# Performance work log

Hardware: AMD Instinct MI355X
Metric: run time of the kernel (lower is better)

The kernel has to match this reference:

```python
import jax, jax.numpy as jnp
import numpy as np

NUM_HEADS = 12
EPS = 1e-6


def softmax_with_policy(attn, policy, eps=EPS):
    # attn: [B, H, N, N]; policy: [B, N, 1]
    B, H, N, _ = attn.shape
    attn_policy = policy.reshape(B, 1, 1, N)
    eye = jnp.eye(N, dtype=attn_policy.dtype).reshape(1, 1, N, N)
    attn_policy = attn_policy + (1.0 - attn_policy) * eye
    max_att = jnp.max(attn, axis=-1, keepdims=True)
    a = jnp.exp((attn - max_att).astype(jnp.float32)) * attn_policy.astype(jnp.float32)
    a = (a + eps / N) / (jnp.sum(a, axis=-1, keepdims=True) + eps)
    return a.astype(attn.dtype)


def setup_inputs() -> dict:
    key = jax.random.key(0)
    k1, k2, k3 = jax.random.split(key, 3)
    B, N, C = 16, 1024, 768
    x = jax.random.normal(k1, (B, N, C), dtype=jnp.float32)
    policy = jax.random.uniform(k2, (B, N, 1), dtype=jnp.float32)
    w_qkv = jax.random.normal(k3, (3 * C, C), dtype=jnp.float32) * (C ** -0.5)
    w_proj = jax.random.normal(jax.random.fold_in(key, 7), (C, C), dtype=jnp.float32) * (C ** -0.5)
    b_proj = jnp.zeros((C,), dtype=jnp.float32)
    return {"x": x, "policy": policy, "w_qkv": w_qkv, "w_proj": w_proj, "b_proj": b_proj, "sampler": 0}


def reference(x, policy, w_qkv, w_proj, b_proj, sampler):
    B, N, C = x.shape
    H = NUM_HEADS
    hd = C // H
    scale = hd ** -0.5
    qkv = (x @ w_qkv.T).reshape(B, N, 3, H, hd)
    qkv = jnp.transpose(qkv, (2, 0, 3, 1, 4))  # [3, B, H, N, hd]
    q, k, v = qkv[0], qkv[1], qkv[2]
    attn = jnp.einsum('bhnd,bhmd->bhnm', q, k) * scale
    attn = softmax_with_policy(attn, policy)
    out = jnp.einsum('bhnm,bhmd->bhnd', attn, v)
    out = jnp.transpose(out, (0, 2, 1, 3)).reshape(B, N, C)
    return out @ w_proj.T + b_proj
```

## Files before the change

kernel.cpp:

```cpp
#include <hip/hip_runtime.h>


#define NB 16
#define NN 1024
#define NC 768
#define NH 12
#define HD 64
#define NM (NB*NN)
#define QKVC (3*NC)
#define QSCALE 0.18033688011112042f
#define PSTR 68

typedef _Float16 f16;
typedef _Float16 f16x8 __attribute__((ext_vector_type(8)));
typedef _Float16 f16x4 __attribute__((ext_vector_type(4)));
typedef __fp16 fp16x2 __attribute__((ext_vector_type(2)));
typedef float f32x4 __attribute__((ext_vector_type(4)));

#if __has_builtin(__builtin_amdgcn_exp2f)
#define EXP2(x) __builtin_amdgcn_exp2f(x)
#else
#define EXP2(x) exp2f(x)
#endif

#define MFMA16(a,b,c) __builtin_amdgcn_mfma_f32_16x16x32_f16((a),(b),(c),0,0,0)
#define SCHED_FENCE() __builtin_amdgcn_sched_barrier(0)

__device__ inline f16x8 as_f16x8(uint4 u){
  union { uint4 u; f16x8 h; } v; v.u = u; return v.h;
}

__device__ inline void gl_lds16(const f16* g, f16* l){
  __builtin_amdgcn_global_load_lds(
      (const __attribute__((address_space(1))) void*)g,
      (__attribute__((address_space(3))) void*)l, 16, 0, 0);
}

#define CVT_N1 (NM*NC/4)
#define CVT_N2 (QKVC*NC/4)
#define CVT_N3 (NC*NC/4)
__global__ void cvt_all(const float* __restrict__ x, const float* __restrict__ wq,
                        const float* __restrict__ wp, f16* __restrict__ xh,
                        f16* __restrict__ wqh, f16* __restrict__ wph){
  int i = blockIdx.x*blockDim.x + threadIdx.x;
  const float* in; f16* out; int j;
  if (i < CVT_N1){ in = x; out = xh; j = i; }
  else if (i < CVT_N1 + CVT_N2){ in = wq; out = wqh; j = i - CVT_N1; }
  else { in = wp; out = wph; j = i - CVT_N1 - CVT_N2; }
  float4 v = ((const float4*)in)[j];
  f16x4 h; h[0]=(f16)v.x; h[1]=(f16)v.y; h[2]=(f16)v.z; h[3]=(f16)v.w;
  ((f16x4*)out)[j] = h;
}

#define GEMM_STAGE(SRC_A, SRC_B, BUF, BK)                                     \
  _Pragma("unroll")                                                           \
  for (int r = 0; r < 2; r++){                                                \
    int row = r*64 + row0;                                                    \
    gl_lds16(SRC_A + (size_t)(R0 + row)*NC + (BK) + kc0, sA[BUF] + r*2048 + w*512); \
    gl_lds16(SRC_B + (size_t)(C0 + row)*NC + (BK) + kc0, sB[BUF] + r*2048 + w*512); \
  }

#define GEMM_PIPELINE(SRC_A, SRC_B)                                           \
  GEMM_STAGE(SRC_A, SRC_B, 0, 0);                                             \
  GEMM_STAGE(SRC_A, SRC_B, 1, 32);                                            \
  _Pragma("unroll 1")                                                         \
  for (int kt = 0; kt < 24; kt++){                                            \
    const int cur = kt % 3;                                                   \
    if (kt < 22){                                                             \
      GEMM_STAGE(SRC_A, SRC_B, (kt+2) % 3, (kt+2)*32);                        \
      asm volatile("s_waitcnt vmcnt(8)" ::: "memory");                        \
    } else if (kt == 22){                                                     \
      asm volatile("s_waitcnt vmcnt(4)" ::: "memory");                        \
    } else {                                                                  \
      asm volatile("s_waitcnt vmcnt(0)" ::: "memory");                        \
    }                                                                         \
    SCHED_FENCE();                                                            \
    __builtin_amdgcn_s_barrier();                                             \
    SCHED_FENCE();                                                            \
    f16x8 af[4], bf[4];                                                       \
    _Pragma("unroll")                                                         \
    for (int mt = 0; mt < 4; mt++)                                            \
      af[mt] = as_f16x8(*(const uint4*)(sA[cur] + (wr*64 + mt*16 + lr)*32 + quad*8)); \
    _Pragma("unroll")                                                         \
    for (int nt = 0; nt < 4; nt++)                                            \
      bf[nt] = as_f16x8(*(const uint4*)(sB[cur] + (wc*64 + nt*16 + lr)*32 + quad*8)); \
    __builtin_amdgcn_s_setprio(1);                                            \
    _Pragma("unroll")                                                         \
    for (int mt = 0; mt < 4; mt++)                                            \
      _Pragma("unroll")                                                       \
      for (int nt = 0; nt < 4; nt++)                                          \
        acc[mt][nt] = MFMA16(af[mt], bf[nt], acc[mt][nt]);                    \
    __builtin_amdgcn_s_setprio(0);                                            \
    SCHED_FENCE();                                                            \
    __builtin_amdgcn_s_barrier();                                             \
    SCHED_FENCE();                                                            \
  }

__launch_bounds__(256)
__global__ void gemm_qkv(const f16* __restrict__ X, const f16* __restrict__ W,
                         f16* __restrict__ Q, f16* __restrict__ K, f16* __restrict__ VT){
  __shared__ f16 sA[3][128*32];
  __shared__ f16 sB[3][128*32];
  const int R0 = blockIdx.y*128, C0 = blockIdx.x*128;
  const int t = threadIdx.x;
  const int w = t >> 6, l = t & 63, quad = l >> 4, lr = l & 15;
  const int wr = w >> 1, wc = w & 1;
  const int row0 = t >> 2, kc0 = (t & 3)*8;
  f32x4 acc[4][4] = {};
  GEMM_PIPELINE(X, W);
  const int type = C0 / NC;
#pragma unroll
  for (int nt = 0; nt < 4; nt++){
    int colg = C0 + wc*64 + nt*16 + lr;
    int rem  = colg - type*NC;
    int hh = rem >> 6, d = rem & 63;
#pragma unroll
    for (int mt = 0; mt < 4; mt++)
#pragma unroll
      for (int i = 0; i < 4; i++){
        int row = R0 + wr*64 + mt*16 + quad*4 + i;
        int bb = row >> 10, np = row & 1023;
        int bh = bb*NH + hh;
        float a = acc[mt][nt][i];
        if (type == 0)      Q[(bh << 16) + (np << 6) + d] = (f16)(a * QSCALE);
        else if (type == 1) K[(bh << 16) + (np << 6) + d] = (f16)a;
        else                VT[(bh << 16) + (d << 10) + np] = (f16)a;
      }
  }
}

__global__ void vsum_kernel(const f16* __restrict__ VT, float* __restrict__ vsum){
  int bh = blockIdx.x;
  int t = threadIdx.x;
  int row = t >> 2, part = t & 3;
  const uint4* p = (const uint4*)(VT + ((size_t)bh << 16) + row*NN + part*256);
  float s = 0.f;
#pragma unroll
  for (int i = 0; i < 32; i++){
    f16x8 v = as_f16x8(p[i]);
#pragma unroll
    for (int j = 0; j < 8; j++) s += (float)v[j];
  }
  __shared__ float sR[64][4];
  sR[row][part] = s;
  __syncthreads();
  if (t < 64) vsum[bh*64 + t] = sR[t][0] + sR[t][1] + sR[t][2] + sR[t][3];
}

#define STAGE(BUF, KEY0H)                                                     \
  _Pragma("unroll")                                                           \
  for (int j = 0; j < 2; j++){                                                \
    const int s_  = j*256 + t;                                                \
    const int r_  = s_ >> 3;                                                  \
    const int sl_ = (s_ & 7) ^ (r_ & 7);                                      \
    f16* du_ = (f16*)&sK[BUF][(j*256 + (t & 192))*8];                         \
    f16* dv_ = (f16*)&sVT[BUF][(j*256 + (t & 192))*8];                        \
    gl_lds16(Kg  + (size_t)((KEY0H) + r_)*HD + sl_*8, du_);                   \
    gl_lds16(VTg + (size_t)r_*NN + (KEY0H) + sl_*8,   dv_);                   \
  }

__launch_bounds__(256, 3)
__global__ void attn_kernel(const f16* __restrict__ Q, const f16* __restrict__ K,
                            const f16* __restrict__ VT, const float* __restrict__ policy,
                            const float* __restrict__ vsum, f16* __restrict__ O){
  __shared__ f16 sK[2][4096];
  __shared__ f16 sVT[2][4096];
  __shared__ f16 sP[4][2][16][PSTR];
  __shared__ float sPol[1024];

  const int blk = blockIdx.x;
  const int bh = blk % (NB*NH);
  const int qt = blk / (NB*NH);
  const int b = bh / NH;
  const size_t base = (size_t)bh << 16;

  const int t = threadIdx.x;
  const int w = t >> 6, l = t & 63, quad = l >> 4, lr = l & 15;
  const int q0 = qt*128 + w*32;
  const int qrow = q0 + lr;
  const int h = bh - b*NH;
  const int xr = lr & 7;
  const int kx0 = (quad ^ xr)*8;
  const int kx1 = ((4 + quad) ^ xr)*8;

  *(float4*)&sPol[t*4] = *(const float4*)(policy + b*NN + t*4);

  f16x8 qf[2][2];
#pragma unroll
  for (int tq = 0; tq < 2; tq++)
#pragma unroll
    for (int hf = 0; hf < 2; hf++)
      qf[tq][hf] = as_f16x8(*(const uint4*)(Q + base + (size_t)(q0 + tq*16 + lr)*HD + hf*32 + quad*8));

  float vs[4];
#pragma unroll
  for (int nt = 0; nt < 4; nt++) vs[nt] = vsum[bh*64 + nt*16 + lr];

  f16x8 ones;
#pragma unroll
  for (int j = 0; j < 8; j++) ones[j] = (f16)1.0f;

  float m_run[2] = {-INFINITY, -INFINITY};
  f32x4 acc_l[2] = {};
  f32x4 o[2][4] = {};

  const f16* Kg  = K + base;
  const f16* VTg = VT + base;

  STAGE(0, 0);
  asm volatile("s_waitcnt vmcnt(0) lgkmcnt(0)" ::: "memory");
  SCHED_FENCE();
  __builtin_amdgcn_s_barrier();
  SCHED_FENCE();

#pragma unroll 1
  for (int hs = 0; hs < 16; hs++){
    const int cur = hs & 1;
    const int key0h = hs*64;
    if (hs < 15){
      STAGE(cur^1, key0h + 64);
      asm volatile("s_waitcnt vmcnt(4)" ::: "memory");
    } else {
      asm volatile("s_waitcnt vmcnt(0)" ::: "memory");
    }
    SCHED_FENCE();
    __builtin_amdgcn_s_barrier();
    SCHED_FENCE();

    const f16* sKc = (const f16*)sK[cur];
    const f16* sVc = (const f16*)sVT[cur];

    f32x4 accA[4], accB[4];
#pragma unroll
    for (int ct = 0; ct < 4; ct++){ accA[ct] = (f32x4){0,0,0,0}; accB[ct] = (f32x4){0,0,0,0}; }
    __builtin_amdgcn_s_setprio(1);
#pragma unroll
    for (int ct = 0; ct < 4; ct++){
      const f16* kp = sKc + (ct*16 + lr)*64;
      f16x8 k0 = as_f16x8(*(const uint4*)(kp + kx0));
      f16x8 k1 = as_f16x8(*(const uint4*)(kp + kx1));
      accA[ct] = MFMA16(k0, qf[0][0], accA[ct]);
      accA[ct] = MFMA16(k1, qf[0][1], accA[ct]);
      accB[ct] = MFMA16(k0, qf[1][0], accB[ct]);
      accB[ct] = MFMA16(k1, qf[1][1], accB[ct]);
    }
    __builtin_amdgcn_s_setprio(0);

    {
      float mA = m_run[0], mB = m_run[1];
      const bool diag = (hs == 2*qt + (w >> 1));
      if (!diag){
#pragma unroll
        for (int ct = 0; ct < 4; ct++){
          const int kb = ct*16 + quad*4;
          float4 pol4 = *(const float4*)&sPol[key0h + kb];
          const float* p4 = (const float*)&pol4;
          mA = fmaxf(mA, fmaxf(fmaxf(accA[ct][0], accA[ct][1]), fmaxf(accA[ct][2], accA[ct][3])));
          mB = fmaxf(mB, fmaxf(fmaxf(accB[ct][0], accB[ct][1]), fmaxf(accB[ct][2], accB[ct][3])));
          union { f16x4 v; fp16x2 h[2]; } uA, uB;
          uA.h[0] = __builtin_amdgcn_cvt_pkrtz(EXP2(accA[ct][0])*p4[0], EXP2(accA[ct][1])*p4[1]);
          uA.h[1] = __builtin_amdgcn_cvt_pkrtz(EXP2(accA[ct][2])*p4[2], EXP2(accA[ct][3])*p4[3]);
          uB.h[0] = __builtin_amdgcn_cvt_pkrtz(EXP2(accB[ct][0])*p4[0], EXP2(accB[ct][1])*p4[1]);
          uB.h[1] = __builtin_amdgcn_cvt_pkrtz(EXP2(accB[ct][2])*p4[2], EXP2(accB[ct][3])*p4[3]);
          *(f16x4*)&sP[w][0][lr][kb] = uA.v;
          *(f16x4*)&sP[w][1][lr][kb] = uB.v;
        }
      } else {
#pragma unroll
        for (int ct = 0; ct < 4; ct++){
          const int kb = ct*16 + quad*4;
          float4 pol4 = *(const float4*)&sPol[key0h + kb];
          const float* p4 = (const float*)&pol4;
          float eA[4], eB[4];
#pragma unroll
          for (int i2 = 0; i2 < 4; i2++){
            int kg = key0h + kb + i2;
            float polA = (kg == qrow)      ? 1.0f : p4[i2];
            float polB = (kg == qrow + 16) ? 1.0f : p4[i2];
            mA = fmaxf(mA, accA[ct][i2]); mB = fmaxf(mB, accB[ct][i2]);
            eA[i2] = EXP2(accA[ct][i2]) * polA;
            eB[i2] = EXP2(accB[ct][i2]) * polB;
          }
          union { f16x4 v; fp16x2 h[2]; } uA, uB;
          uA.h[0] = __builtin_amdgcn_cvt_pkrtz(eA[0], eA[1]);
          uA.h[1] = __builtin_amdgcn_cvt_pkrtz(eA[2], eA[3]);
          uB.h[0] = __builtin_amdgcn_cvt_pkrtz(eB[0], eB[1]);
          uB.h[1] = __builtin_amdgcn_cvt_pkrtz(eB[2], eB[3]);
          *(f16x4*)&sP[w][0][lr][kb] = uA.v;
          *(f16x4*)&sP[w][1][lr][kb] = uB.v;
        }
      }
      m_run[0] = mA; m_run[1] = mB;
    }

    __builtin_amdgcn_s_setprio(1);
#pragma unroll
    for (int s8g = 0; s8g < 2; s8g++){
      f16x8 pfA = as_f16x8(*(const uint4*)&sP[w][0][lr][s8g*32 + quad*8]);
      f16x8 pfB = as_f16x8(*(const uint4*)&sP[w][1][lr][s8g*32 + quad*8]);
      acc_l[0] = MFMA16(pfA, ones, acc_l[0]);
      acc_l[1] = MFMA16(pfB, ones, acc_l[1]);
      const int sx = ((s8g*4 + quad) ^ xr)*8;
#pragma unroll
      for (int nt = 0; nt < 4; nt++){
        f16x8 vf = as_f16x8(*(const uint4*)(sVc + (nt*16 + lr)*64 + sx));
        o[0][nt] = MFMA16(pfA, vf, o[0][nt]);
        o[1][nt] = MFMA16(pfB, vf, o[1][nt]);
      }
    }
    __builtin_amdgcn_s_setprio(0);
    SCHED_FENCE();
    __builtin_amdgcn_s_barrier();
    SCHED_FENCE();
  }

#pragma unroll
  for (int tq = 0; tq < 2; tq++){
    float mq = m_run[tq];
    mq = fmaxf(mq, __shfl_xor(mq, 16));
    mq = fmaxf(mq, __shfl_xor(mq, 32));
#pragma unroll
    for (int i = 0; i < 4; i++){
      float mi = __shfl(mq, quad*4 + i);
      float E  = EXP2(mi);
      float li = acc_l[tq][i];
      float inv = 1.0f / (li + 1e-6f*E);
      float ec  = (1e-6f/1024.0f)*E;
      int row = q0 + tq*16 + quad*4 + i;
      f16* op = O + (size_t)(b*NN + row)*NC + h*HD;
#pragma unroll
      for (int nt = 0; nt < 4; nt++)
        op[nt*16 + lr] = (f16)((o[tq][nt][i] + ec*vs[nt]) * inv);
    }
  }
}

__launch_bounds__(256)
__global__ void gemm_proj(const f16* __restrict__ A, const f16* __restrict__ W,
                          const float* __restrict__ bias, float* __restrict__ out){
  __shared__ f16 sA[3][128*32];
  __shared__ f16 sB[3][128*32];
  const int R0 = blockIdx.y*128, C0 = blockIdx.x*128;
  const int t = threadIdx.x;
  const int w = t >> 6, l = t & 63, quad = l >> 4, lr = l & 15;
  const int wr = w >> 1, wc = w & 1;
  const int row0 = t >> 2, kc0 = (t & 3)*8;
  f32x4 acc[4][4] = {};
  GEMM_PIPELINE(A, W);
#pragma unroll
  for (int nt = 0; nt < 4; nt++){
    int colg = C0 + wc*64 + nt*16 + lr;
    float bv = bias[colg];
#pragma unroll
    for (int mt = 0; mt < 4; mt++)
#pragma unroll
      for (int i = 0; i < 4; i++){
        int row = R0 + wr*64 + mt*16 + quad*4 + i;
        out[(size_t)row*NC + colg] = acc[mt][nt][i] + bv;
      }
  }
}

extern "C" void kernel_launch(void* const* d_in, const int* in_sizes, int n_in,
                              void* d_out, int out_size, void* d_ws, size_t ws_size,
                              hipStream_t stream) {
  const float* x      = (const float*)d_in[0];
  const float* policy = (const float*)d_in[1];
  const float* w_qkv  = (const float*)d_in[2];
  const float* w_proj = (const float*)d_in[3];
  const float* b_proj = (const float*)d_in[4];
  float* out = (float*)d_out;

  f16* x_h     = (f16*)d_ws;
  f16* wqkv_h  = x_h + (size_t)NM*NC;
  f16* wproj_h = wqkv_h + (size_t)QKVC*NC;
  f16* q_h     = wproj_h + (size_t)NC*NC;
  f16* k_h     = q_h + (size_t)NM*NC;
  f16* vt_h    = k_h + (size_t)NM*NC;
  float* vsum_f = (float*)(vt_h + (size_t)NM*NC);
  f16* attn_h  = x_h;

  cvt_all<<<(CVT_N1+CVT_N2+CVT_N3)/256, 256, 0, stream>>>(x, w_qkv, w_proj, x_h, wqkv_h, wproj_h);

  gemm_qkv<<<dim3(QKVC/128, NM/128), 256, 0, stream>>>(x_h, wqkv_h, q_h, k_h, vt_h);

  vsum_kernel<<<dim3(NB*NH), 256, 0, stream>>>(vt_h, vsum_f);

  attn_kernel<<<dim3(NB*NH*(NN/128)), 256, 0, stream>>>(q_h, k_h, vt_h, policy, vsum_f, attn_h);

  gemm_proj<<<dim3(NC/128, NM/128), 256, 0, stream>>>(attn_h, wproj_h, b_proj, out);
}
```

Measured before the change: 345.9 us.

## Use 256x256 GEMM tiles with 512 threads, XOR-swizzled LDS, and split-stage prefetch

Both the QKV and projection GEMMs move from 128x128 tiles with 256 threads and a 3-stage BK=32 pipeline to 256x256 tiles with 512 threads. The new loop is a double-buffered BK=64 pipeline whose A and B prefetches are interleaved with the two K-halves of MFMA work. LDS rows are XOR-swizzled to avoid bank conflicts. The larger tile raises arithmetic intensity and reuse per block, but each block now holds 128 accumulator floats per thread, needs 128KB of LDS, and the grid has far fewer blocks (e.g. 3x64 for the projection GEMM), which risks poor CU utilisation.

New measurement: 348.1 us. About the same (+0.6%).

```diff
diff --git a/kernel.cpp b/kernel.cpp
--- a/kernel.cpp
+++ b/kernel.cpp
@@ -52,62 +52,80 @@
   ((f16x4*)out)[j] = h;
 }
 
-#define GEMM_STAGE(SRC_A, SRC_B, BUF, BK)                                     \
+#define G_STAGE(SRC, DSTB, KT, RC0)                                           \
   _Pragma("unroll")                                                           \
-  for (int r = 0; r < 2; r++){                                                \
-    int row = r*64 + row0;                                                    \
-    gl_lds16(SRC_A + (size_t)(R0 + row)*NC + (BK) + kc0, sA[BUF] + r*2048 + w*512); \
-    gl_lds16(SRC_B + (size_t)(C0 + row)*NC + (BK) + kc0, sB[BUF] + r*2048 + w*512); \
-  }
-
-#define GEMM_PIPELINE(SRC_A, SRC_B)                                           \
-  GEMM_STAGE(SRC_A, SRC_B, 0, 0);                                             \
-  GEMM_STAGE(SRC_A, SRC_B, 1, 32);                                            \
+  for (int j = 0; j < 4; j++){                                                \
+    const int r_ = j*64 + (t >> 3);                                           \
+    gl_lds16(SRC + (size_t)((RC0) + r_)*NC + (KT) + sslot*8,                  \
+             (DSTB) + j*4096 + wv*512);                                       \
+  }
+
+#define GEMM256_PIPELINE(SRC_A, SRC_B)                                        \
+  G_STAGE(SRC_A, sA, 0, R0);                                                  \
+  G_STAGE(SRC_B, sB, 0, C0);                                                  \
   _Pragma("unroll 1")                                                         \
-  for (int kt = 0; kt < 24; kt++){                                            \
-    const int cur = kt % 3;                                                   \
-    if (kt < 22){                                                             \
-      GEMM_STAGE(SRC_A, SRC_B, (kt+2) % 3, (kt+2)*32);                        \
-      asm volatile("s_waitcnt vmcnt(8)" ::: "memory");                        \
-    } else if (kt == 22){                                                     \
-      asm volatile("s_waitcnt vmcnt(4)" ::: "memory");                        \
-    } else {                                                                  \
-      asm volatile("s_waitcnt vmcnt(0)" ::: "memory");                        \
-    }                                                                         \
+  for (int tt = 0; tt < 12; tt++){                                            \
+    const int cur = tt & 1;                                                   \
+    asm volatile("s_waitcnt vmcnt(0)" ::: "memory");      \
     SCHED_FENCE();                                                            \
-    __builtin_amdgcn_s_barrier();                                             \
-    SCHED_FENCE();                                                            \
-    f16x8 af[4], bf[4];                                                       \
-    _Pragma("unroll")                                                         \
-    for (int mt = 0; mt < 4; mt++)                                            \
-      af[mt] = as_f16x8(*(const uint4*)(sA[cur] + (wr*64 + mt*16 + lr)*32 + quad*8)); \
-    _Pragma("unroll")                                                         \
-    for (int nt = 0; nt < 4; nt++)                                            \
-      bf[nt] = as_f16x8(*(const uint4*)(sB[cur] + (wc*64 + nt*16 + lr)*32 + quad*8)); \
-    __builtin_amdgcn_s_setprio(1);                                            \
-    _Pragma("unroll")                                                         \
-    for (int mt = 0; mt < 4; mt++)                                            \
+    __builtin_amdgcn_s_barrier();                      \
+    SCHED_FENCE();                                     \
+    const f16* A_ = sA + (cur ? 16384 : 0);                                   \
+    const f16* B_ = sB + (cur ? 16384 : 0);                                   \
+    f16* An_ = sA + (cur ? 0 : 16384);                                        \
+    f16* Bn_ = sB + (cur ? 0 : 16384);                                        \
+    if (tt < 11){ G_STAGE(SRC_A, An_, (tt+1)*64, R0); }                       \
+    {                                                                         \
+      f16x8 bf[4];                                                            \
       _Pragma("unroll")                                                       \
       for (int nt = 0; nt < 4; nt++)                                          \
-        acc[mt][nt] = MFMA16(af[mt], bf[nt], acc[mt][nt]);                    \
-    __builtin_amdgcn_s_setprio(0);                                            \
-    SCHED_FENCE();                                                            \
-    __builtin_amdgcn_s_barrier();                                             \
-    SCHED_FENCE();                                                            \
-  }
-
-__launch_bounds__(256)
+        bf[nt] = as_f16x8(*(const uint4*)(B_ + (wc*64 + nt*16 + lr)*64 + kxA0)); \
+      __builtin_amdgcn_s_setprio(1);                                          \
+      _Pragma("unroll")                                                       \
+      for (int mt = 0; mt < 8; mt++){                                         \
+        f16x8 af = as_f16x8(*(const uint4*)(A_ + (wr*128 + mt*16 + lr)*64 + kxA0)); \
+        _Pragma("unroll")                                                     \
+        for (int nt = 0; nt < 4; nt++)                                        \
+          acc[mt][nt] = MFMA16(af, bf[nt], acc[mt][nt]);                      \
+      }                                                                       \
+      __builtin_amdgcn_s_setprio(0);                                          \
+    }                                                                         \
+    if (tt < 11){ G_STAGE(SRC_B, Bn_, (tt+1)*64, C0); }                       \
+    {                                                                         \
+      f16x8 bf[4];                                                            \
+      _Pragma("unroll")                                                       \
+      for (int nt = 0; nt < 4; nt++)                                          \
+        bf[nt] = as_f16x8(*(const uint4*)(B_ + (wc*64 + nt*16 + lr)*64 + kxA1)); \
+      __builtin_amdgcn_s_setprio(1);                                          \
+      _Pragma("unroll")                                                       \
+      for (int mt = 0; mt < 8; mt++){                                         \
+        f16x8 af = as_f16x8(*(const uint4*)(A_ + (wr*128 + mt*16 + lr)*64 + kxA1)); \
+        _Pragma("unroll")                                                     \
+        for (int nt = 0; nt < 4; nt++)                                        \
+          acc[mt][nt] = MFMA16(af, bf[nt], acc[mt][nt]);                      \
+      }                                                                       \
+      __builtin_amdgcn_s_setprio(0);                                          \
+    }                                                                         \
+  }
+
+#define GEMM256_PREAMBLE                                                      \
+  const int R0 = blockIdx.y*256, C0 = blockIdx.x*256;                         \
+  const int t = threadIdx.x;                                                  \
+  const int wv = t >> 6, l = t & 63, quad = l >> 4, lr = l & 15;              \
+  const int wr = wv >> 2, wc = wv & 3;                                        \
+  const int sslot = (t & 7) ^ ((t >> 3) & 7);                                 \
+  const int xr = lr & 7;                                                      \
+  const int kxA0 = (quad ^ xr)*8;                                             \
+  const int kxA1 = ((4 + quad) ^ xr)*8;                                       \
+  f32x4 acc[8][4] = {};
+
+__launch_bounds__(512, 2)
 __global__ void gemm_qkv(const f16* __restrict__ X, const f16* __restrict__ W,
                          f16* __restrict__ Q, f16* __restrict__ K, f16* __restrict__ VT){
-  __shared__ f16 sA[3][128*32];
-  __shared__ f16 sB[3][128*32];
-  const int R0 = blockIdx.y*128, C0 = blockIdx.x*128;
-  const int t = threadIdx.x;
-  const int w = t >> 6, l = t & 63, quad = l >> 4, lr = l & 15;
-  const int wr = w >> 1, wc = w & 1;
-  const int row0 = t >> 2, kc0 = (t & 3)*8;
-  f32x4 acc[4][4] = {};
-  GEMM_PIPELINE(X, W);
+  __shared__ f16 sA[2*16384];
+  __shared__ f16 sB[2*16384];
+  GEMM256_PREAMBLE;
+  GEMM256_PIPELINE(X, W);
   const int type = C0 / NC;
 #pragma unroll
   for (int nt = 0; nt < 4; nt++){
@@ -115,10 +133,10 @@
     int rem  = colg - type*NC;
     int hh = rem >> 6, d = rem & 63;
 #pragma unroll
-    for (int mt = 0; mt < 4; mt++)
+    for (int mt = 0; mt < 8; mt++)
 #pragma unroll
       for (int i = 0; i < 4; i++){
-        int row = R0 + wr*64 + mt*16 + quad*4 + i;
+        int row = R0 + wr*128 + mt*16 + quad*4 + i;
         int bb = row >> 10, np = row & 1023;
         int bh = bb*NH + hh;
         float a = acc[mt][nt][i];
@@ -335,27 +353,22 @@
   }
 }
 
-__launch_bounds__(256)
+__launch_bounds__(512, 2)
 __global__ void gemm_proj(const f16* __restrict__ A, const f16* __restrict__ W,
                           const float* __restrict__ bias, float* __restrict__ out){
-  __shared__ f16 sA[3][128*32];
-  __shared__ f16 sB[3][128*32];
-  const int R0 = blockIdx.y*128, C0 = blockIdx.x*128;
-  const int t = threadIdx.x;
-  const int w = t >> 6, l = t & 63, quad = l >> 4, lr = l & 15;
-  const int wr = w >> 1, wc = w & 1;
-  const int row0 = t >> 2, kc0 = (t & 3)*8;
-  f32x4 acc[4][4] = {};
-  GEMM_PIPELINE(A, W);
+  __shared__ f16 sA[2*16384];
+  __shared__ f16 sB[2*16384];
+  GEMM256_PREAMBLE;
+  GEMM256_PIPELINE(A, W);
 #pragma unroll
   for (int nt = 0; nt < 4; nt++){
     int colg = C0 + wc*64 + nt*16 + lr;
     float bv = bias[colg];
 #pragma unroll
-    for (int mt = 0; mt < 4; mt++)
+    for (int mt = 0; mt < 8; mt++)
 #pragma unroll
       for (int i = 0; i < 4; i++){
-        int row = R0 + wr*64 + mt*16 + quad*4 + i;
+        int row = R0 + wr*128 + mt*16 + quad*4 + i;
         out[(size_t)row*NC + colg] = acc[mt][nt][i] + bv;
       }
   }
@@ -382,11 +395,11 @@
 
   cvt_all<<<(CVT_N1+CVT_N2+CVT_N3)/256, 256, 0, stream>>>(x, w_qkv, w_proj, x_h, wqkv_h, wproj_h);
 
-  gemm_qkv<<<dim3(QKVC/128, NM/128), 256, 0, stream>>>(x_h, wqkv_h, q_h, k_h, vt_h);
+  gemm_qkv<<<dim3(QKVC/256, NM/256), 512, 0, stream>>>(x_h, wqkv_h, q_h, k_h, vt_h);
 
   vsum_kernel<<<dim3(NB*NH), 256, 0, stream>>>(vt_h, vsum_f);
 
   attn_kernel<<<dim3(NB*NH*(NN/128)), 256, 0, stream>>>(q_h, k_h, vt_h, policy, vsum_f, attn_h);
 
-  gemm_proj<<<dim3(NC/128, NM/128), 256, 0, stream>>>(attn_h, wproj_h, b_proj, out);
-}
+  gemm_proj<<<dim3(NC/256, NM/256), 512, 0, stream>>>(attn_h, wproj_h, b_proj, out);
+}
```
